# Performance work log

Measured on AMD Instinct MI355X. Metric: run time of the kernel, lower is better.

The kernel has to match this reference:

```python
import jax, jax.numpy as jnp
import numpy as np

B, T, I, H, NC = 128, 512, 128, 512, 100


def setup_inputs() -> dict:
    key = jax.random.key(0)
    ks = jax.random.split(key, 16)
    x = jax.random.randint(ks[0], (B, T, 1), 0, NC + 1)
    # embedding table with padding row 0 zeroed (padding_idx=0)
    emb = (jax.random.normal(ks[1], (NC + 1, I)) * 1.0).at[0].set(0.0)
    # kaiming_normal_ fan_out, sigmoid nonlinearity -> std = 1/sqrt(fan_out)
    sx = 1.0 / np.sqrt(H)
    sc = 1.0 / np.sqrt(H)
    sp = 1.0 / np.sqrt(NC)
    return {
        "x": x,
        "emb": emb,
        "Wfx": jax.random.normal(ks[2], (I, H)) * sx,
        "Wfc": jax.random.normal(ks[3], (H, H)) * sc,
        "bf": jnp.zeros((H,)),
        "Wix": jax.random.normal(ks[4], (I, H)) * sx,
        "Wic": jax.random.normal(ks[5], (H, H)) * sc,
        "bi": jnp.zeros((H,)),
        "Wox": jax.random.normal(ks[6], (I, H)) * sx,
        "Woc": jax.random.normal(ks[7], (H, H)) * sc,
        "bo": jnp.zeros((H,)),
        "Wcx": jax.random.normal(ks[8], (I, H)) * sx,
        "bc": jnp.zeros((H,)),
        "Wph": jax.random.normal(ks[9], (H, NC)) * sp,
        "bp": jnp.zeros((NC,)),
    }


def reference(x, emb, Wfx, Wfc, bf, Wix, Wic, bi, Wox, Woc, bo, Wcx, bc, Wph, bp):
    idx = x[:, :, 0]                      # [B,T] int indices
    xe = emb[idx]                         # [B,T,I] embedded inputs
    h_dim = Wfc.shape[0]
    # Fuse the four input-side GEMMs into one, hoisted out of the recurrence.
    Wx = jnp.concatenate([Wfx, Wix, Wox, Wcx], axis=1)   # [I,4H]
    bx = jnp.concatenate([bf, bi, bo, bc])               # [4H]
    xg = jnp.einsum('bti,ih->bth', xe, Wx) + bx          # [B,T,4H]
    # Fuse the three peephole (cell-state) GEMMs into one per step.
    Wc = jnp.concatenate([Wfc, Wic, Woc], axis=1)        # [H,3H]
    reset = (idx > 0).astype(xg.dtype)                   # [B,T]

    def step(carry, inp):
        C, h = carry
        g, r = inp                        # g: [B,4H], r: [B]
        cg = C @ Wc                       # [B,3H]
        f = jax.nn.sigmoid(g[:, :h_dim] + cg[:, :h_dim])
        i = jax.nn.sigmoid(g[:, h_dim:2 * h_dim] + cg[:, h_dim:2 * h_dim])
        o = jax.nn.sigmoid(g[:, 2 * h_dim:3 * h_dim] + cg[:, 2 * h_dim:])
        c_tilde = jax.nn.sigmoid(g[:, 3 * h_dim:])        # note: sigmoid, not tanh (per source)
        Cn = (c_tilde * i + C * f) * r[:, None]           # reset on padding tokens
        hn = jnp.tanh(Cn) * o
        return (Cn, hn), None

    bsz = xg.shape[0]
    init = (jnp.zeros((bsz, h_dim), xg.dtype), jnp.zeros((bsz, h_dim), xg.dtype))
    xs = (jnp.swapaxes(xg, 0, 1), jnp.swapaxes(reset, 0, 1))  # time-major
    (Cf, hf), _ = jax.lax.scan(step, init, xs)
    p = hf @ Wph + bp                     # [B,num_classes]
    return jax.nn.log_softmax(p, axis=1)
```

## Files before the change

kernel.cpp:

```cpp
#include <hip/hip_runtime.h>
#include <hip/hip_bf16.h>
#include <stdint.h>

#define HD   512
#define ID   128
#define NCLS 100
#define TT   512
#define BB   128
#define NEMB 101
#define THR  512

#define NGRPB 64
#define GWGB  4
#define RPGB  2
#define COLSB 128
#define NGRPF 32
#define GWGF  8
#define RPGF  4
#define COLSF 64

#define CPAD 640
#define CBW  260
#define PSTF 5
#define PSTB 3

#define WS_FLAG 0
#define WS_BAR  4096
#define WS_G    65536
#define WS_C0   (1u * 1024 * 1024)
#define WS_C1   (WS_C0 + 262144)
#define WS_HFB  (WS_C1 + 262144)
#define NBARU   4096

using bf16 = __hip_bfloat16;

__device__ __forceinline__ float b2f(bf16 v) { return __bfloat162float(v); }
__device__ __forceinline__ float sigf(float x) { return 1.0f / (1.0f + expf(-x)); }

__device__ __forceinline__ float cld(const float* p) {
    return __hip_atomic_load(p, __ATOMIC_RELAXED, __HIP_MEMORY_SCOPE_AGENT);
}
__device__ __forceinline__ void cst(float* p, float v) {
    __hip_atomic_store(p, v, __ATOMIC_RELAXED, __HIP_MEMORY_SCOPE_AGENT);
}
__device__ __forceinline__ uint64_t cld8(const float* p) {
    return __hip_atomic_load((const uint64_t*)p, __ATOMIC_RELAXED,
                             __HIP_MEMORY_SCOPE_AGENT);
}

__device__ __forceinline__ uint32_t pkbf(float x, float y) {
    uint32_t u;
    asm("v_cvt_pk_bf16_f32 %0, %1, %2" : "=v"(u) : "v"(x), "v"(y));
    return u;
}
#define DOT2(acc, w, c) \
    asm("v_dot2_f32_bf16 %0, %1, %2, %0" : "+v"(acc) : "v"(w), "v"(c))

template <bool BF>
__device__ __forceinline__ float ldv(const void* p, int i) {
    if constexpr (BF) return b2f(((const bf16*)p)[i]);
    else              return ((const float*)p)[i];
}

__device__ __forceinline__ int cpi(int h) { return (h >> 4) * 20 + (h & 15); }

__device__ __forceinline__ void gbarrier(unsigned* cnt, unsigned* iter, int gwg) {
    __syncthreads();
    if (threadIdx.x == 0) {
        __hip_atomic_fetch_add(cnt, 1u, __ATOMIC_RELAXED, __HIP_MEMORY_SCOPE_AGENT);
        const unsigned tgt = (*iter + 1u) * (unsigned)gwg;
        while (__hip_atomic_load(cnt, __ATOMIC_RELAXED, __HIP_MEMORY_SCOPE_AGENT) < tgt)
            ;
    }
    ++*iter;
    __syncthreads();
}

__global__ void init_k(const uint32_t* __restrict__ emb_raw,
                       int* __restrict__ flag, unsigned* __restrict__ bars) {
    const int t = threadIdx.x;
    for (int k = t; k < NBARU; k += 1024) bars[k] = 0u;
    if (t == 0) {
        uint32_t acc = 0;
        for (int i = 64; i < 128; ++i) acc |= emb_raw[i];
        *flag = (acc == 0u) ? 0 : 1;
    }
}

template <bool BF>
__global__ void build_G(const int* __restrict__ flag,
                        const void* __restrict__ emb,
                        const void* __restrict__ Wfx, const void* __restrict__ Wix,
                        const void* __restrict__ Wox, const void* __restrict__ Wcx,
                        const void* __restrict__ bfv, const void* __restrict__ biv,
                        const void* __restrict__ bov, const void* __restrict__ bcv,
                        float* __restrict__ G) {
    if (*flag != (BF ? 1 : 0)) return;
    const int c   = blockIdx.x;
    const int j   = blockIdx.y * 256 + threadIdx.x;
    const int q   = j >> 9;
    const int col = j & 511;
    const void* W  = (q == 0) ? Wfx : (q == 1) ? Wix : (q == 2) ? Wox : Wcx;
    const void* bv = (q == 0) ? bfv : (q == 1) ? biv : (q == 2) ? bov : bcv;
    float acc = ldv<BF>(bv, col);
    for (int i = 0; i < ID; ++i)
        acc += ldv<BF>(emb, c * ID + i) * ldv<BF>(W, i * HD + col);
    if (q == 3) acc = sigf(acc);
    G[c * 2048 + j] = acc;
}

template <bool BF>
__global__ __launch_bounds__(THR, 2) void recur_bs(
    const int* __restrict__ flag, const int* __restrict__ x,
    const float* __restrict__ G,
    const void* __restrict__ Wfc, const void* __restrict__ Wic,
    const void* __restrict__ Woc,
    float* __restrict__ C0, float* __restrict__ C1,
    float* __restrict__ Hfb, unsigned* __restrict__ bars)
{
    if (*flag != (BF ? 1 : 0)) return;

    __shared__ __align__(16) float Cs[RPGF * CPAD];
    __shared__ __align__(8)  float2 part2[2048 * PSTF];
    __shared__ int idx[RPGF * TT];
    __shared__ int lz[RPGF];

    const int blk = blockIdx.x;
    const int tid = threadIdx.x;
    unsigned bi = 0;

    if constexpr (BF) {
        const int grp   = blk >> 2;
        const int rank  = blk & 3;
        const int r0    = grp * RPGB;
        const int h0    = rank * COLSB;
        const int cp    = tid & 31;
        const int chunk = tid >> 5;
        unsigned* bar = bars + grp * 32;

        idx[tid]       = x[r0 * TT + tid];
        idx[tid + 512] = x[r0 * TT + tid + 512];
        if (tid < RPGB) lz[tid] = -1;
        __syncthreads();
        #pragma unroll
        for (int r = 0; r < RPGB; ++r)
            if (idx[r * TT + tid] == 0) atomicMax(&lz[r], tid);
        __syncthreads();
        int t0 = TT;
        #pragma unroll
        for (int r = 0; r < RPGB; ++r) t0 = min(t0, lz[r] + 1);

        const uint16_t* Wfr = (const uint16_t*)Wfc;
        const uint16_t* Wir = (const uint16_t*)Wic;
        uint32_t wf0[16], wf1[16], wf2[16], wf3[16];
        uint32_t wi0[16], wi1[16], wi2[16], wi3[16];
        #pragma unroll
        for (int p = 0; p < 16; ++p) {
            const int hp = chunk * 32 + 2 * p;
            const int b0 = hp * HD + h0 + cp, b1 = (hp + 1) * HD + h0 + cp;
            wf0[p] = (uint32_t)Wfr[b0]      | ((uint32_t)Wfr[b1]      << 16);
            wf1[p] = (uint32_t)Wfr[b0 + 32] | ((uint32_t)Wfr[b1 + 32] << 16);
            wf2[p] = (uint32_t)Wfr[b0 + 64] | ((uint32_t)Wfr[b1 + 64] << 16);
            wf3[p] = (uint32_t)Wfr[b0 + 96] | ((uint32_t)Wfr[b1 + 96] << 16);
            wi0[p] = (uint32_t)Wir[b0]      | ((uint32_t)Wir[b1]      << 16);
            wi1[p] = (uint32_t)Wir[b0 + 32] | ((uint32_t)Wir[b1 + 32] << 16);
            wi2[p] = (uint32_t)Wir[b0 + 64] | ((uint32_t)Wir[b1 + 64] << 16);
            wi3[p] = (uint32_t)Wir[b0 + 96] | ((uint32_t)Wir[b1 + 96] << 16);
        }
        #pragma unroll
        for (int p = 0; p < 16; ++p)
            asm volatile("" : "+v"(wf0[p]), "+v"(wf1[p]), "+v"(wf2[p]), "+v"(wf3[p]),
                              "+v"(wi0[p]), "+v"(wi1[p]), "+v"(wi2[p]), "+v"(wi3[p]));

        const bool isUpd = (tid < COLSB * RPGB);
        const int uc = tid & 127, ur = tid >> 7;

        if (isUpd) {
            cst(&C0[(r0 + ur) * HD + h0 + uc], 0.0f);
            cst(&C1[(r0 + ur) * HD + h0 + uc], 0.0f);
        }
        gbarrier(bar, &bi, GWGB);

        float Creg = 0.0f;
        uint32_t* Cb = (uint32_t*)Cs;
        const int srow = tid >> 8;
        const int spr  = tid & 255;

        for (int t = t0; t < TT; ++t) {
            #pragma unroll
            for (int p = 0; p < 16; ++p)
                asm volatile("" : "+v"(wf0[p]), "+v"(wf1[p]), "+v"(wf2[p]), "+v"(wf3[p]),
                                  "+v"(wi0[p]), "+v"(wi1[p]), "+v"(wi2[p]), "+v"(wi3[p]));

            const float* cur = (t & 1) ? C1 : C0;
            float*       nxt = (t & 1) ? C0 : C1;

            float gf = 0.f, gi = 0.f, sgc = 0.f;
            int cl = 1;
            if (isUpd) {
                cl = idx[ur * TT + t];
                const float* Gr = G + cl * 2048;
                gf  = Gr[h0 + uc];
                gi  = Gr[512 + h0 + uc];
                sgc = Gr[1536 + h0 + uc];
            }

            {
                const uint64_t a = cld8(cur + (r0 + srow) * HD + 2 * spr);
                Cb[srow * CBW + spr] = pkbf(__uint_as_float((uint32_t)a),
                                            __uint_as_float((uint32_t)(a >> 32)));
            }
            __syncthreads();

            float f0[RPGB], f1[RPGB], f2[RPGB], f3[RPGB];
            float i0[RPGB], i1[RPGB], i2[RPGB], i3[RPGB];
            #pragma unroll
            for (int r = 0; r < RPGB; ++r) {
                f0[r] = 0.f; f1[r] = 0.f; f2[r] = 0.f; f3[r] = 0.f;
                i0[r] = 0.f; i1[r] = 0.f; i2[r] = 0.f; i3[r] = 0.f;
            }
            {
                const int cb = chunk * 16;
                #pragma unroll
                for (int hh = 0; hh < 4; ++hh) {
                    #pragma unroll
                    for (int r = 0; r < RPGB; ++r) {
                        const uint4 cv = *reinterpret_cast<const uint4*>(
                            Cb + r * CBW + cb + 4 * hh);
                        const int p = 4 * hh;
                        DOT2(f0[r], wf0[p + 0], cv.x); DOT2(f0[r], wf0[p + 1], cv.y);
                        DOT2(f0[r], wf0[p + 2], cv.z); DOT2(f0[r], wf0[p + 3], cv.w);
                        DOT2(f1[r], wf1[p + 0], cv.x); DOT2(f1[r], wf1[p + 1], cv.y);
                        DOT2(f1[r], wf1[p + 2], cv.z); DOT2(f1[r], wf1[p + 3], cv.w);
                        DOT2(f2[r], wf2[p + 0], cv.x); DOT2(f2[r], wf2[p + 1], cv.y);
                        DOT2(f2[r], wf2[p + 2], cv.z); DOT2(f2[r], wf2[p + 3], cv.w);
                        DOT2(f3[r], wf3[p + 0], cv.x); DOT2(f3[r], wf3[p + 1], cv.y);
                        DOT2(f3[r], wf3[p + 2], cv.z); DOT2(f3[r], wf3[p + 3], cv.w);
                        DOT2(i0[r], wi0[p + 0], cv.x); DOT2(i0[r], wi0[p + 1], cv.y);
                        DOT2(i0[r], wi0[p + 2], cv.z); DOT2(i0[r], wi0[p + 3], cv.w);
                        DOT2(i1[r], wi1[p + 0], cv.x); DOT2(i1[r], wi1[p + 1], cv.y);
                        DOT2(i1[r], wi1[p + 2], cv.z); DOT2(i1[r], wi1[p + 3], cv.w);
                        DOT2(i2[r], wi2[p + 0], cv.x); DOT2(i2[r], wi2[p + 1], cv.y);
                        DOT2(i2[r], wi2[p + 2], cv.z); DOT2(i2[r], wi2[p + 3], cv.w);
                        DOT2(i3[r], wi3[p + 0], cv.x); DOT2(i3[r], wi3[p + 1], cv.y);
                        DOT2(i3[r], wi3[p + 2], cv.z); DOT2(i3[r], wi3[p + 3], cv.w);
                    }
                }
            }
            {
                float2* p0 = part2 + (chunk * 128 + cp)      * PSTB;
                float2* p1 = part2 + (chunk * 128 + cp + 32) * PSTB;
                float2* p2 = part2 + (chunk * 128 + cp + 64) * PSTB;
                float2* p3 = part2 + (chunk * 128 + cp + 96) * PSTB;
                #pragma unroll
                for (int r = 0; r < RPGB; ++r) {
                    p0[r] = make_float2(f0[r], i0[r]);
                    p1[r] = make_float2(f1[r], i1[r]);
                    p2[r] = make_float2(f2[r], i2[r]);
                    p3[r] = make_float2(f3[r], i3[r]);
                }
            }
            __syncthreads();

            if (isUpd) {
                float df = 0.f, di = 0.f;
                #pragma unroll
                for (int ch = 0; ch < 16; ++ch) {
                    const float2 v = part2[(ch * 128 + uc) * PSTB + ur];
                    df += v.x;
                    di += v.y;
                }
                float Cn = sgc * sigf(gi + di) + Creg * sigf(gf + df);
                Cn = (cl > 0) ? Cn : 0.0f;
                Creg = Cn;
                cst(&nxt[(r0 + ur) * HD + h0 + uc], Cn);
            }
            gbarrier(bar, &bi, GWGB);
        }

        {
            const float v0 = cld(C1 + (r0 + 0) * HD + tid);
            const float v1 = cld(C1 + (r0 + 1) * HD + tid);
            const int pe = cpi(tid);
            Cs[0 * CPAD + pe] = v0;
            Cs[1 * CPAD + pe] = v1;
            __syncthreads();

            const int oc = tid & 127, och = tid >> 7;
            float ao0 = 0.f, ao1 = 0.f;
            #pragma unroll 4
            for (int k = 0; k < 128; ++k) {
                const int hp  = och * 128 + k;
                const int hpp = cpi(hp);
                const float wo = ldv<BF>(Woc, hp * HD + h0 + oc);
                ao0 += wo * Cs[0 * CPAD + hpp];
                ao1 += wo * Cs[1 * CPAD + hpp];
            }
            part2[(och * 128 + oc) * PSTB] = make_float2(ao0, ao1);
            __syncthreads();
            if (isUpd) {
                float s = 0.f;
                #pragma unroll
                for (int ch = 0; ch < 4; ++ch) {
                    const float2 v = part2[(ch * 128 + uc) * PSTB];
                    s += ur ? v.y : v.x;
                }
                const int cl2 = idx[ur * TT + TT - 1];
                const float o = sigf(G[cl2 * 2048 + 1024 + h0 + uc] + s);
                Hfb[(r0 + ur) * HD + h0 + uc] = tanhf(Creg) * o;
            }
        }
    } else {
        const int grp   = blk >> 3;
        const int rank  = blk & 7;
        const int r0    = grp * RPGF;
        const int h0    = rank * COLSF;
        const int cp    = tid & 15;
        const int chunk = tid >> 4;
        unsigned* bar = bars + grp * 32;

        idx[tid]        = x[r0 * TT + tid];
        idx[tid + 512]  = x[r0 * TT + tid + 512];
        idx[tid + 1024] = x[r0 * TT + tid + 1024];
        idx[tid + 1536] = x[r0 * TT + tid + 1536];
        if (tid < RPGF) lz[tid] = -1;
        __syncthreads();
        #pragma unroll
        for (int r = 0; r < RPGF; ++r)
            if (idx[r * TT + tid] == 0) atomicMax(&lz[r], tid);
        __syncthreads();
        int t0 = TT;
        #pragma unroll
        for (int r = 0; r < RPGF; ++r) t0 = min(t0, lz[r] + 1);

        float wf0[16], wf1[16], wf2[16], wf3[16];
        float wi0[16], wi1[16], wi2[16], wi3[16];
        #pragma unroll
        for (int k = 0; k < 16; ++k) {
            const int hp = chunk * 16 + k;
            wf0[k] = ldv<BF>(Wfc, hp * HD + h0 + cp);
            wf1[k] = ldv<BF>(Wfc, hp * HD + h0 + cp + 16);
            wf2[k] = ldv<BF>(Wfc, hp * HD + h0 + cp + 32);
            wf3[k] = ldv<BF>(Wfc, hp * HD + h0 + cp + 48);
            wi0[k] = ldv<BF>(Wic, hp * HD + h0 + cp);
            wi1[k] = ldv<BF>(Wic, hp * HD + h0 + cp + 16);
            wi2[k] = ldv<BF>(Wic, hp * HD + h0 + cp + 32);
            wi3[k] = ldv<BF>(Wic, hp * HD + h0 + cp + 48);
        }
        #pragma unroll
        for (int k = 0; k < 16; ++k)
            asm volatile("" : "+v"(wf0[k]), "+v"(wf1[k]), "+v"(wf2[k]), "+v"(wf3[k]),
                              "+v"(wi0[k]), "+v"(wi1[k]), "+v"(wi2[k]), "+v"(wi3[k]));

        const bool isUpd = (tid < COLSF * RPGF);
        const int uc = tid & 63, ur = tid >> 6;
        const int pe = cpi(tid);

        if (isUpd) {
            cst(&C0[(r0 + ur) * HD + h0 + uc], 0.0f);
            cst(&C1[(r0 + ur) * HD + h0 + uc], 0.0f);
        }
        gbarrier(bar, &bi, GWGF);

        float Creg = 0.0f;
        for (int t = t0; t < TT; ++t) {
            #pragma unroll
            for (int k = 0; k < 16; ++k)
                asm volatile("" : "+v"(wf0[k]), "+v"(wf1[k]), "+v"(wf2[k]), "+v"(wf3[k]),
                                  "+v"(wi0[k]), "+v"(wi1[k]), "+v"(wi2[k]), "+v"(wi3[k]));

            const float* cur = (t & 1) ? C1 : C0;
            float*       nxt = (t & 1) ? C0 : C1;

            float gf = 0.f, gi = 0.f, sgc = 0.f;
            int cl = 1;
            if (isUpd) {
                cl = idx[ur * TT + t];
                const float* Gr = G + cl * 2048;
                gf  = Gr[h0 + uc];
                gi  = Gr[512 + h0 + uc];
                sgc = Gr[1536 + h0 + uc];
            }

            {
                const float v0 = cld(cur + (r0 + 0) * HD + tid);
                const float v1 = cld(cur + (r0 + 1) * HD + tid);
                const float v2 = cld(cur + (r0 + 2) * HD + tid);
                const float v3 = cld(cur + (r0 + 3) * HD + tid);
                Cs[0 * CPAD + pe] = v0;
                Cs[1 * CPAD + pe] = v1;
                Cs[2 * CPAD + pe] = v2;
                Cs[3 * CPAD + pe] = v3;
            }
            __syncthreads();

            float f0[RPGF], f1[RPGF], f2[RPGF], f3[RPGF];
            float i0[RPGF], i1[RPGF], i2[RPGF], i3[RPGF];
            #pragma unroll
            for (int r = 0; r < RPGF; ++r) {
                f0[r] = 0.f; f1[r] = 0.f; f2[r] = 0.f; f3[r] = 0.f;
                i0[r] = 0.f; i1[r] = 0.f; i2[r] = 0.f; i3[r] = 0.f;
            }
            {
                const int cb = chunk * 5;
                #pragma unroll
                for (int j = 0; j < 4; ++j) {
                    #pragma unroll
                    for (int r = 0; r < RPGF; ++r) {
                        const float4 cv = reinterpret_cast<const float4*>(
                            Cs + r * CPAD)[cb + j];
                        f0[r] += wf0[4*j]*cv.x + wf0[4*j+1]*cv.y + wf0[4*j+2]*cv.z + wf0[4*j+3]*cv.w;
                        f1[r] += wf1[4*j]*cv.x + wf1[4*j+1]*cv.y + wf1[4*j+2]*cv.z + wf1[4*j+3]*cv.w;
                        f2[r] += wf2[4*j]*cv.x + wf2[4*j+1]*cv.y + wf2[4*j+2]*cv.z + wf2[4*j+3]*cv.w;
                        f3[r] += wf3[4*j]*cv.x + wf3[4*j+1]*cv.y + wf3[4*j+2]*cv.z + wf3[4*j+3]*cv.w;
                        i0[r] += wi0[4*j]*cv.x + wi0[4*j+1]*cv.y + wi0[4*j+2]*cv.z + wi0[4*j+3]*cv.w;
                        i1[r] += wi1[4*j]*cv.x + wi1[4*j+1]*cv.y + wi1[4*j+2]*cv.z + wi1[4*j+3]*cv.w;
                        i2[r] += wi2[4*j]*cv.x + wi2[4*j+1]*cv.y + wi2[4*j+2]*cv.z + wi2[4*j+3]*cv.w;
                        i3[r] += wi3[4*j]*cv.x + wi3[4*j+1]*cv.y + wi3[4*j+2]*cv.z + wi3[4*j+3]*cv.w;
                    }
                }
            }
            {
                float2* p0 = part2 + (chunk * 64 + cp)      * PSTF;
                float2* p1 = part2 + (chunk * 64 + cp + 16) * PSTF;
                float2* p2 = part2 + (chunk * 64 + cp + 32) * PSTF;
                float2* p3 = part2 + (chunk * 64 + cp + 48) * PSTF;
                #pragma unroll
                for (int r = 0; r < RPGF; ++r) {
                    p0[r] = make_float2(f0[r], i0[r]);
                    p1[r] = make_float2(f1[r], i1[r]);
                    p2[r] = make_float2(f2[r], i2[r]);
                    p3[r] = make_float2(f3[r], i3[r]);
                }
            }
            __syncthreads();

            if (isUpd) {
                float df = 0.f, di = 0.f;
                #pragma unroll
                for (int ch = 0; ch < 32; ++ch) {
                    const float2 v = part2[(ch * 64 + uc) * PSTF + ur];
                    df += v.x;
                    di += v.y;
                }
                float Cn = sgc * sigf(gi + di) + Creg * sigf(gf + df);
                Cn = (cl > 0) ? Cn : 0.0f;
                Creg = Cn;
                cst(&nxt[(r0 + ur) * HD + h0 + uc], Cn);
            }
            gbarrier(bar, &bi, GWGF);
        }

        {
            const float v0 = cld(C1 + (r0 + 0) * HD + tid);
            const float v1 = cld(C1 + (r0 + 1) * HD + tid);
            const float v2 = cld(C1 + (r0 + 2) * HD + tid);
            const float v3 = cld(C1 + (r0 + 3) * HD + tid);
            Cs[0 * CPAD + pe] = v0;
            Cs[1 * CPAD + pe] = v1;
            Cs[2 * CPAD + pe] = v2;
            Cs[3 * CPAD + pe] = v3;
            __syncthreads();

            const int oc = tid & 63, och = tid >> 6;
            float ao[RPGF];
            #pragma unroll
            for (int r = 0; r < RPGF; ++r) ao[r] = 0.0f;
            #pragma unroll 4
            for (int k = 0; k < 64; ++k) {
                const int hp = och * 64 + k;
                const int hpp = cpi(hp);
                const float wo = ldv<BF>(Woc, hp * HD + h0 + oc);
                #pragma unroll
                for (int r = 0; r < RPGF; ++r)
                    ao[r] += wo * Cs[r * CPAD + hpp];
            }
            {
                float2* pp = part2 + (och * 64 + oc) * PSTF;
                #pragma unroll
                for (int r2 = 0; r2 < RPGF / 2; ++r2)
                    pp[r2] = make_float2(ao[2 * r2], ao[2 * r2 + 1]);
            }
            __syncthreads();
            if (isUpd) {
                float s = 0.f;
                #pragma unroll
                for (int ch = 0; ch < 8; ++ch) {
                    const float2 v = part2[(ch * 64 + uc) * PSTF + (ur >> 1)];
                    s += (ur & 1) ? v.y : v.x;
                }
                const int cl2 = idx[ur * TT + TT - 1];
                const float o = sigf(G[cl2 * 2048 + 1024 + h0 + uc] + s);
                Hfb[(r0 + ur) * HD + h0 + uc] = tanhf(Creg) * o;
            }
        }
    }
}

template <bool BF>
__global__ __launch_bounds__(128) void proj(
    const int* __restrict__ flag, const float* __restrict__ Hfb,
    const void* __restrict__ Wph, const void* __restrict__ bp,
    void* __restrict__ out)
{
    if (*flag != (BF ? 1 : 0)) return;
    __shared__ __align__(16) float hv[HD];
    __shared__ float p_s[NCLS];
    __shared__ float lse_s;
    const int b   = blockIdx.x;
    const int tid = threadIdx.x;

    reinterpret_cast<float4*>(hv)[tid] =
        reinterpret_cast<const float4*>(Hfb + b * HD)[tid];
    __syncthreads();

    if (tid < NCLS) {
        float p = ldv<BF>(bp, tid);
        for (int h = 0; h < HD; ++h)
            p += hv[h] * ldv<BF>(Wph, h * NCLS + tid);
        p_s[tid] = p;
    }
    __syncthreads();
    if (tid == 0) {
        float m = -1e30f;
        for (int n = 0; n < NCLS; ++n) m = fmaxf(m, p_s[n]);
        float sum = 0.0f;
        for (int n = 0; n < NCLS; ++n) sum += expf(p_s[n] - m);
        lse_s = m + logf(sum);
    }
    __syncthreads();
    if (tid < NCLS) {
        const float v = p_s[tid] - lse_s;
        if constexpr (BF) ((bf16*)out)[b * NCLS + tid] = __float2bfloat16(v);
        else              ((float*)out)[b * NCLS + tid] = v;
    }
}

extern "C" void kernel_launch(void* const* d_in, const int* in_sizes, int n_in,
                              void* d_out, int out_size, void* d_ws, size_t ws_size,
                              hipStream_t stream) {
    const int*  x   = (const int*)d_in[0];
    const void* emb = d_in[1];
    const void* Wfx = d_in[2];
    const void* Wfc = d_in[3];
    const void* bfv = d_in[4];
    const void* Wix = d_in[5];
    const void* Wic = d_in[6];
    const void* biv = d_in[7];
    const void* Wox = d_in[8];
    const void* Woc = d_in[9];
    const void* bov = d_in[10];
    const void* Wcx = d_in[11];
    const void* bcv = d_in[12];
    const void* Wph = d_in[13];
    const void* bp  = d_in[14];

    int*      flag = (int*)((char*)d_ws + WS_FLAG);
    unsigned* bars = (unsigned*)((char*)d_ws + WS_BAR);
    float*    G    = (float*)((char*)d_ws + WS_G);
    float*    C0   = (float*)((char*)d_ws + WS_C0);
    float*    C1   = (float*)((char*)d_ws + WS_C1);
    float*    Hfb  = (float*)((char*)d_ws + WS_HFB);

    init_k<<<1, 1024, 0, stream>>>((const uint32_t*)emb, flag, bars);

    build_G<false><<<dim3(NEMB, 8), 256, 0, stream>>>(flag, emb, Wfx, Wix, Wox, Wcx,
                                                      bfv, biv, bov, bcv, G);
    build_G<true ><<<dim3(NEMB, 8), 256, 0, stream>>>(flag, emb, Wfx, Wix, Wox, Wcx,
                                                      bfv, biv, bov, bcv, G);

    {
        void* args[] = {(void*)&flag, (void*)&x, (void*)&G,
                        (void*)&Wfc, (void*)&Wic, (void*)&Woc,
                        (void*)&C0, (void*)&C1, (void*)&Hfb, (void*)&bars};
        hipLaunchCooperativeKernel((const void*)recur_bs<false>, dim3(256), dim3(THR),
                                   args, 0, stream);
        hipLaunchCooperativeKernel((const void*)recur_bs<true>, dim3(256), dim3(THR),
                                   args, 0, stream);
    }

    proj<false><<<BB, 128, 0, stream>>>(flag, Hfb, Wph, bp, d_out);
    proj<true ><<<BB, 128, 0, stream>>>(flag, Hfb, Wph, bp, d_out);
}
```

Baseline: 1.599 ms.

## Replace per-step group barrier with step-tagged bf16 cell-state flags in BF path

In the bf16 recurrence path, each cell-state word now packs the bf16 value in the high half and the timestep in the low half. Consumers spin on an atomic 64-bit load until both words carry the expected step tag, which removes the global atomic barrier per timestep. Init zeroes the C buffers on the device, and the final C is read from the shared bf16 copy instead of global memory. The catch is that the final Woc projection now uses bf16-rounded C, and correctness relies on double buffering, which a lagging reader must not overrun; the 16-bit step tag would wrap only above 65535 steps.

Result: no change. 1.593 ms (-0.3%).

```diff
diff --git a/kernel.cpp b/kernel.cpp
--- a/kernel.cpp
+++ b/kernel.cpp
@@ -31,6 +31,7 @@
 #define WS_C1   (WS_C0 + 262144)
 #define WS_HFB  (WS_C1 + 262144)
 #define NBARU   4096
+#define NCU     65536
 
 using bf16 = __hip_bfloat16;
 
@@ -43,9 +44,11 @@
 __device__ __forceinline__ void cst(float* p, float v) {
     __hip_atomic_store(p, v, __ATOMIC_RELAXED, __HIP_MEMORY_SCOPE_AGENT);
 }
-__device__ __forceinline__ uint64_t cld8(const float* p) {
-    return __hip_atomic_load((const uint64_t*)p, __ATOMIC_RELAXED,
-                             __HIP_MEMORY_SCOPE_AGENT);
+__device__ __forceinline__ void cstu(uint32_t* p, uint32_t v) {
+    __hip_atomic_store(p, v, __ATOMIC_RELAXED, __HIP_MEMORY_SCOPE_AGENT);
+}
+__device__ __forceinline__ uint64_t cldu8(const uint64_t* p) {
+    return __hip_atomic_load(p, __ATOMIC_RELAXED, __HIP_MEMORY_SCOPE_AGENT);
 }
 
 __device__ __forceinline__ uint32_t pkbf(float x, float y) {
@@ -77,9 +80,11 @@
 }
 
 __global__ void init_k(const uint32_t* __restrict__ emb_raw,
-                       int* __restrict__ flag, unsigned* __restrict__ bars) {
-    const int t = threadIdx.x;
-    for (int k = t; k < NBARU; k += 1024) bars[k] = 0u;
+                       int* __restrict__ flag, unsigned* __restrict__ bars,
+                       uint32_t* __restrict__ c0, uint32_t* __restrict__ c1) {
+    const int t = blockIdx.x * 1024 + threadIdx.x;
+    for (int k = t; k < NBARU; k += 8192) bars[k] = 0u;
+    for (int k = t; k < NCU; k += 8192) { c0[k] = 0u; c1[k] = 0u; }
     if (t == 0) {
         uint32_t acc = 0;
         for (int i = 64; i < 128; ++i) acc |= emb_raw[i];
@@ -121,6 +126,7 @@
     if (*flag != (BF ? 1 : 0)) return;
 
     __shared__ __align__(16) float Cs[RPGF * CPAD];
+    __shared__ __align__(16) uint32_t CbS[RPGB * CBW];
     __shared__ __align__(8)  float2 part2[2048 * PSTF];
     __shared__ int idx[RPGF * TT];
     __shared__ int lz[RPGF];
@@ -136,10 +142,10 @@
         const int h0    = rank * COLSB;
         const int cp    = tid & 31;
         const int chunk = tid >> 5;
-        unsigned* bar = bars + grp * 32;
 
         idx[tid]       = x[r0 * TT + tid];
         idx[tid + 512] = x[r0 * TT + tid + 512];
+        for (int k = tid; k < RPGB * CBW; k += THR) CbS[k] = 0u;
         if (tid < RPGB) lz[tid] = -1;
         __syncthreads();
         #pragma unroll
@@ -175,14 +181,12 @@
         const bool isUpd = (tid < COLSB * RPGB);
         const int uc = tid & 127, ur = tid >> 7;
 
-        if (isUpd) {
-            cst(&C0[(r0 + ur) * HD + h0 + uc], 0.0f);
-            cst(&C1[(r0 + ur) * HD + h0 + uc], 0.0f);
-        }
-        gbarrier(bar, &bi, GWGB);
+        if (isUpd && t0 > 0) {
+            uint32_t* b0 = (uint32_t*)((t0 & 1) ? C1 : C0);
+            cstu(b0 + (r0 + ur) * HD + h0 + uc, (uint32_t)t0 & 0xFFFFu);
+        }
 
         float Creg = 0.0f;
-        uint32_t* Cb = (uint32_t*)Cs;
         const int srow = tid >> 8;
         const int spr  = tid & 255;
 
@@ -192,8 +196,8 @@
                 asm volatile("" : "+v"(wf0[p]), "+v"(wf1[p]), "+v"(wf2[p]), "+v"(wf3[p]),
                                   "+v"(wi0[p]), "+v"(wi1[p]), "+v"(wi2[p]), "+v"(wi3[p]));
 
-            const float* cur = (t & 1) ? C1 : C0;
-            float*       nxt = (t & 1) ? C0 : C1;
+            const uint32_t* curT = (const uint32_t*)((t & 1) ? C1 : C0);
+            uint32_t*       nxtT = (uint32_t*)((t & 1) ? C0 : C1);
 
             float gf = 0.f, gi = 0.f, sgc = 0.f;
             int cl = 1;
@@ -206,9 +210,17 @@
             }
 
             {
-                const uint64_t a = cld8(cur + (r0 + srow) * HD + 2 * spr);
-                Cb[srow * CBW + spr] = pkbf(__uint_as_float((uint32_t)a),
-                                            __uint_as_float((uint32_t)(a >> 32)));
+                const uint64_t* src = (const uint64_t*)(
+                    curT + (r0 + srow) * HD + 2 * spr);
+                const uint32_t exp = (uint32_t)t & 0xFFFFu;
+                uint32_t w0, w1;
+                for (;;) {
+                    const uint64_t d = cldu8(src);
+                    w0 = (uint32_t)d;
+                    w1 = (uint32_t)(d >> 32);
+                    if ((((w0 ^ exp) | (w1 ^ exp)) & 0xFFFFu) == 0u) break;
+                }
+                CbS[srow * CBW + spr] = (w0 >> 16) | (w1 & 0xFFFF0000u);
             }
             __syncthreads();
 
@@ -226,7 +238,7 @@
                     #pragma unroll
                     for (int r = 0; r < RPGB; ++r) {
                         const uint4 cv = *reinterpret_cast<const uint4*>(
-                            Cb + r * CBW + cb + 4 * hh);
+                            CbS + r * CBW + cb + 4 * hh);
                         const int p = 4 * hh;
                         DOT2(f0[r], wf0[p + 0], cv.x); DOT2(f0[r], wf0[p + 1], cv.y);
                         DOT2(f0[r], wf0[p + 2], cv.z); DOT2(f0[r], wf0[p + 3], cv.w);
@@ -273,17 +285,17 @@
                 float Cn = sgc * sigf(gi + di) + Creg * sigf(gf + df);
                 Cn = (cl > 0) ? Cn : 0.0f;
                 Creg = Cn;
-                cst(&nxt[(r0 + ur) * HD + h0 + uc], Cn);
-            }
-            gbarrier(bar, &bi, GWGB);
+                const uint32_t vb = pkbf(Cn, Cn);
+                cstu(nxtT + (r0 + ur) * HD + h0 + uc,
+                     (vb << 16) | ((uint32_t)(t + 1) & 0xFFFFu));
+            }
         }
 
         {
-            const float v0 = cld(C1 + (r0 + 0) * HD + tid);
-            const float v1 = cld(C1 + (r0 + 1) * HD + tid);
-            const int pe = cpi(tid);
-            Cs[0 * CPAD + pe] = v0;
-            Cs[1 * CPAD + pe] = v1;
+            const int rr = tid >> 8, wi = tid & 255;
+            const uint32_t w = CbS[rr * CBW + wi];
+            Cs[rr * CPAD + cpi(2 * wi)]     = __uint_as_float((w & 0xFFFFu) << 16);
+            Cs[rr * CPAD + cpi(2 * wi + 1)] = __uint_as_float(w & 0xFFFF0000u);
             __syncthreads();
 
             const int oc = tid & 127, och = tid >> 7;
@@ -562,7 +574,8 @@
     float*    C1   = (float*)((char*)d_ws + WS_C1);
     float*    Hfb  = (float*)((char*)d_ws + WS_HFB);
 
-    init_k<<<1, 1024, 0, stream>>>((const uint32_t*)emb, flag, bars);
+    init_k<<<8, 1024, 0, stream>>>((const uint32_t*)emb, flag, bars,
+                                   (uint32_t*)C0, (uint32_t*)C1);
 
     build_G<false><<<dim3(NEMB, 8), 256, 0, stream>>>(flag, emb, Wfx, Wix, Wox, Wcx,
                                                       bfv, biv, bov, bcv, G);
```
